# Performance work log

Measured on AMD Instinct MI355X. Metric: run time of the kernel, lower is better.

Reference implementation:

```python
import jax, jax.numpy as jnp
import numpy as np

N_NODES = 10000
N_EDGES = 5_000_000
BATCH = 2000


def setup_inputs() -> dict:
    key = jax.random.key(0)
    k1, k2, k3, k4 = jax.random.split(key, 4)
    n, E = N_NODES, N_EDGES
    # valid undirected pairs i < j
    i = jax.random.randint(k1, (E,), 0, n - 1)
    r = jax.random.randint(k2, (E,), 0, n)
    j = i + 1 + r % (n - 1 - i)
    edges = jnp.stack([i, j])  # [2, E], int
    edge_times = jax.random.uniform(k3, (E,), dtype=jnp.float32)
    edge_states = jax.random.randint(k4, (E,), 0, 2)
    return {
        "edges": edges,
        "edge_times": edge_times,
        "edge_states": edge_states,
        "nodes_num": n,
        "batch_size": BATCH,
    }


def _flat_idx(i, j, n):
    # undirected upper-triangular linearization of pair (i, j), i < j
    return i * n - i * (i + 1) // 2 + (j - i - 1)


def reference(edges, edge_times, edge_states, nodes_num, batch_size):
    n = nodes_num
    # -- multinomial(arange(n), batch_size, replacement=False) via Gumbel top-k --
    key = jax.random.key(19)
    w = jnp.arange(n, dtype=jnp.float32)
    logw = jnp.where(w > 0, jnp.log(jnp.maximum(w, 1.0)), -jnp.inf)
    scores = logw + jax.random.gumbel(key, (n,), dtype=jnp.float32)
    _, sel = jax.lax.top_k(scores, batch_size)
    batch_nodes = jnp.sort(sel)

    # -- all combinations (i < j since batch_nodes is sorted) --
    ii, jj = np.triu_indices(batch_size, k=1)  # static shapes
    batch_pairs = jnp.stack([batch_nodes[ii], batch_nodes[jj]])  # [2, P]
    batch_flat = _flat_idx(batch_pairs[0], batch_pairs[1], n)  # ascending

    # -- gather stored edges whose pair index is in the batch --
    edge_flat = _flat_idx(edges[0], edges[1], n)
    order = jnp.argsort(edge_flat)  # jax sort is stable -> matches coalesce order
    edges_sorted = edges[:, order]
    flat_sorted = edge_flat[order]
    times_sorted = edge_times[order]
    states_sorted = edge_states[order]

    pos = jnp.searchsorted(batch_flat, flat_sorted)
    pos = jnp.clip(pos, 0, batch_flat.shape[0] - 1)
    mask = batch_flat[pos] == flat_sorted  # [E] membership of each edge in batch

    batch_edge_times = jnp.where(mask, times_sorted, 0.0)
    batch_states = jnp.where(mask, states_sorted, 0)
    return (batch_nodes, batch_pairs, edges_sorted, batch_edge_times,
            batch_states, mask)
```

## Files before the change

### kernel.cpp

```cpp
#include <hip/hip_runtime.h>
#include <stdint.h>
#include <math.h>

#define N_NODES  10000
#define N_EDGES  5000000
#define BATCH    2000
#define N_PAIRS  1999000

#define OUT_BN      0
#define OUT_PAIRS0  2000
#define OUT_PAIRS1  2001000
#define OUT_ES0     4000000
#define OUT_ES1     9000000
#define OUT_T       14000000
#define OUT_S       19000000
#define OUT_M       24000000

#define WS_KEYS     0
#define WS_SEL      80000
#define WS_BN       120000
#define WS_CNT      128000
#define WS_FILL     168000
#define WS_OFF      208000
#define WS_SCRATCH  248064


#define RPB_LOG  7
#define NB1      79
#define CHUNK    4096
#define NBIN     192
#define NBITSW   313
#define RANK_BLKS 200
#define HIST_BLKS 128

typedef unsigned long long u64;

__device__ __forceinline__ u64 score_key(int w, unsigned bits) {
  const float TINY = 1.17549435e-38f;
  float uf = __uint_as_float((bits >> 9) | 0x3f800000u) - 1.0f;
  float val = fmaxf(TINY, uf + TINY);
  float t1 = (float)log((double)val);
  float gmb = -(float)log((double)(-t1));
  float score = (w > 0) ? ((float)log((double)w) + gmb) : (-INFINITY);
  unsigned fb = __float_as_uint(score);
  unsigned s = (fb & 0x80000000u) ? ~fb : (fb | 0x80000000u);
  unsigned d = ~s;
  return ((u64)d << 32) | (unsigned)w;
}

__device__ __forceinline__ u64 make_key(int v) {
  unsigned ks[3] = {0u, 19u, 0u ^ 19u ^ 0x1BD11BDAu};
  unsigned x0 = 0u + ks[0];
  unsigned x1 = (unsigned)v + ks[1];
  const int R0[4] = {13, 15, 26, 6};
  const int R1[4] = {17, 29, 16, 24};
#pragma unroll
  for (int g = 0; g < 5; ++g) {
    const int* R = (g & 1) ? R1 : R0;
#pragma unroll
    for (int r = 0; r < 4; ++r) {
      x0 += x1;
      x1 = (x1 << R[r]) | (x1 >> (32 - R[r]));
      x1 ^= x0;
    }
    x0 += ks[(g + 1) % 3];
    x1 += ks[(g + 2) % 3] + (unsigned)(g + 1);
  }
  return score_key(v, x0 ^ x1);
}

__global__ void __launch_bounds__(256) k_rankhist(
    int* __restrict__ rankc, int* __restrict__ cnt,
    const int4* __restrict__ e_i4) {
  __shared__ __align__(16) int sh4[N_NODES];
  int tid = threadIdx.x;
  if ((int)blockIdx.x < RANK_BLKS) {
    u64* lk = (u64*)sh4;
    int vblk = blockIdx.x / 5, cblk = blockIdx.x % 5;
    int base = cblk * 2048;
    int lenc = min(2048, N_NODES - base);
    for (int t = tid; t < lenc; t += 256) lk[t] = make_key(base + t);
    __syncthreads();
    int v = vblk * 256 + tid;
    u64 kv = (v < N_NODES) ? make_key(v) : 0;
    int c = 0;
    for (int t = 0; t < lenc; ++t) c += (lk[t] < kv) ? 1 : 0;
    if (v < N_NODES && c) atomicAdd(&rankc[v], c);
  } else {
    int* h = sh4;
    for (int t = tid; t < N_NODES; t += 256) h[t] = 0;
    __syncthreads();
    int hb = blockIdx.x - RANK_BLKS;
    int stride = HIST_BLKS * 256;
    for (int t = hb * 256 + tid; t < N_EDGES / 4; t += stride) {
      int4 r = e_i4[t];
      atomicAdd(&h[r.x], 1);
      atomicAdd(&h[r.y], 1);
      atomicAdd(&h[r.z], 1);
      atomicAdd(&h[r.w], 1);
    }
    __syncthreads();
    for (int t = tid; t < N_NODES; t += 256) {
      int c = h[t];
      if (c) atomicAdd(&cnt[t], c);
    }
  }
}

__global__ void k_scan_all(const int* rankc, int* sel, int* bn, float* outbn,
                           const int* cnt, int* off, int* fill, int* fill1,
                           unsigned* selbits) {
  __shared__ int wsum[16];
  __shared__ unsigned lb[320];
  const int PER = 10;
  int tid = threadIdx.x, lane = tid & 63, wid = tid >> 6;
  int base = tid * PER;
  int svv[PER];
  {
    int s = 0;
#pragma unroll
    for (int k = 0; k < PER; ++k) {
      int i = base + k;
      if (i < N_NODES) {
        int sv = (rankc[i] < BATCH) ? 1 : 0;
        sel[i] = sv;
        svv[k] = sv;
        s += sv;
      } else svv[k] = 0;
    }
    int inc = s;
#pragma unroll
    for (int d = 1; d < 64; d <<= 1) {
      int v = __shfl_up(inc, d, 64);
      if (lane >= d) inc += v;
    }
    if (lane == 63) wsum[wid] = inc;
    __syncthreads();
    int woff = 0;
    for (int w = 0; w < wid; ++w) woff += wsum[w];
    int run = woff + inc - s;
#pragma unroll
    for (int k = 0; k < PER; ++k) {
      int i = base + k;
      if (i < N_NODES && svv[k]) {
        bn[run] = i;
        outbn[run] = (float)i;
        ++run;
      }
    }
  }
  __syncthreads();
  {
    int cv[PER];
    int s = 0;
#pragma unroll
    for (int k = 0; k < PER; ++k) {
      int i = base + k;
      if (i < N_NODES) { cv[k] = cnt[i]; s += cv[k]; } else cv[k] = 0;
    }
    int inc = s;
#pragma unroll
    for (int d = 1; d < 64; d <<= 1) {
      int v = __shfl_up(inc, d, 64);
      if (lane >= d) inc += v;
    }
    if (lane == 63) wsum[wid] = inc;
    __syncthreads();
    int woff = 0;
    for (int w = 0; w < wid; ++w) woff += wsum[w];
    int run = woff + inc - s;
#pragma unroll
    for (int k = 0; k < PER; ++k) {
      int i = base + k;
      if (i < N_NODES) {
        off[i] = run;
        fill[i] = run;
        if ((i & ((1 << RPB_LOG) - 1)) == 0) fill1[i >> RPB_LOG] = run;
        run += cv[k];
      }
    }
    if (tid == 0) off[N_NODES] = N_EDGES;
  }
  __syncthreads();
  if (tid < 320) lb[tid] = 0;
  __syncthreads();
#pragma unroll
  for (int k = 0; k < PER; ++k) {
    int i = base + k;
    if (i < N_NODES && svv[k]) atomicOr(&lb[i >> 5], 1u << (i & 31));
  }
  __syncthreads();
  if (tid < NBITSW) selbits[tid] = lb[tid];
}

__global__ void __launch_bounds__(256) k_pairs_part1(
    const int* __restrict__ e_i, const int* __restrict__ e_j,
    const int* __restrict__ st, int* __restrict__ fill1,
    u64* __restrict__ stage, const int* __restrict__ bn,
    float* __restrict__ outp, int nblk1) {
  __shared__ u64 lkey[CHUNK];
  __shared__ int h[4][NB1];
  __shared__ int bstart[NB1], basec[NB1];
  __shared__ int tcount_s;
  int tid = threadIdx.x, wid = tid >> 6;
  if ((int)blockIdx.x >= nblk1) {
    int p = ((int)blockIdx.x - nblk1) * 256 + tid;
    if (p >= N_PAIRS) return;
    float tf = 2.0f * BATCH - 1.0f;
    float disc = tf * tf - 8.0f * (float)p;
    int ii = (int)((tf - sqrtf(disc)) * 0.5f);
    if (ii < 0) ii = 0;
    if (ii > BATCH - 2) ii = BATCH - 2;
    while (ii > 0 &&
           (long long)ii * (BATCH - 1) - (long long)ii * (ii - 1) / 2 > p) --ii;
    while ((long long)(ii + 1) * (BATCH - 1) - (long long)(ii + 1) * ii / 2 <= p) ++ii;
    long long S = (long long)ii * (BATCH - 1) - (long long)ii * (ii - 1) / 2;
    int jj = ii + 1 + (int)(p - S);
    outp[p] = (float)bn[ii];
    outp[N_PAIRS + p] = (float)bn[jj];
    return;
  }
  int c0 = (int)blockIdx.x * CHUNK;
  int nloc = min(CHUNK, N_EDGES - c0);
  for (int t = tid; t < 4 * NB1; t += 256) ((int*)h)[t] = 0;
  __syncthreads();
  int iv[CHUNK / 256];
  const int4* e_i4 = (const int4*)(e_i + c0);
#pragma unroll
  for (int k = 0; k < CHUNK / 1024; ++k) {
    int q = tid + 256 * k;
    int ebase = 4 * q;
    if (ebase < nloc) {
      int4 r = e_i4[q];
      iv[4 * k + 0] = r.x; iv[4 * k + 1] = r.y;
      iv[4 * k + 2] = r.z; iv[4 * k + 3] = r.w;
      atomicAdd(&h[wid][r.x >> RPB_LOG], 1);
      atomicAdd(&h[wid][r.y >> RPB_LOG], 1);
      atomicAdd(&h[wid][r.z >> RPB_LOG], 1);
      atomicAdd(&h[wid][r.w >> RPB_LOG], 1);
    } else {
      iv[4 * k + 0] = iv[4 * k + 1] = iv[4 * k + 2] = iv[4 * k + 3] = -1;
    }
  }
  __syncthreads();
  if (tid < 64) {
    int a0 = h[0][tid], a1 = h[1][tid], a2 = h[2][tid], a3 = h[3][tid];
    int a = a0 + a1 + a2 + a3;
    int b0 = 0, b1 = 0, b2 = 0, b3 = 0, b = 0;
    if (tid + 64 < NB1) {
      b0 = h[0][tid + 64]; b1 = h[1][tid + 64];
      b2 = h[2][tid + 64]; b3 = h[3][tid + 64];
      b = b0 + b1 + b2 + b3;
    }
    int inc0 = a;
#pragma unroll
    for (int d = 1; d < 64; d <<= 1) {
      int v = __shfl_up(inc0, d, 64);
      if (tid >= d) inc0 += v;
    }
    int t0 = __shfl(inc0, 63, 64);
    int inc1 = b;
#pragma unroll
    for (int d = 1; d < 64; d <<= 1) {
      int v = __shfl_up(inc1, d, 64);
      if (tid >= d) inc1 += v;
    }
    int tot = t0 + __shfl(inc1, 63, 64);
    int e0 = inc0 - a;
    bstart[tid] = e0;
    h[0][tid] = e0;
    h[1][tid] = e0 + a0;
    h[2][tid] = e0 + a0 + a1;
    h[3][tid] = e0 + a0 + a1 + a2;
    basec[tid] = a ? atomicAdd(&fill1[tid], a) : 0;
    if (tid + 64 < NB1) {
      int e1 = t0 + inc1 - b;
      bstart[tid + 64] = e1;
      h[0][tid + 64] = e1;
      h[1][tid + 64] = e1 + b0;
      h[2][tid + 64] = e1 + b0 + b1;
      h[3][tid + 64] = e1 + b0 + b1 + b2;
      basec[tid + 64] = b ? atomicAdd(&fill1[tid + 64], b) : 0;
    }
    if (tid == 0) tcount_s = tot;
  }
  __syncthreads();
  const int4* e_j4 = (const int4*)(e_j + c0);
  const int4* st4 = (const int4*)(st + c0);
#pragma unroll
  for (int k = 0; k < CHUNK / 1024; ++k) {
    int q = tid + 256 * k;
    int ebase = 4 * q;
    if (ebase < nloc) {
      int4 jj = e_j4[q];
      int4 ss = st4[q];
      int js[4] = {jj.x, jj.y, jj.z, jj.w};
      int s4[4] = {ss.x, ss.y, ss.z, ss.w};
#pragma unroll
      for (int c = 0; c < 4; ++c) {
        int i = iv[4 * k + c];
        unsigned e = (unsigned)(c0 + ebase + c);
        int b = i >> RPB_LOG;
        int pos = atomicAdd(&h[wid][b], 1);
        lkey[pos] = ((u64)(unsigned)i << 38) | ((u64)(unsigned)js[c] << 24) |
                    ((u64)e << 1) | (u64)(unsigned)s4[c];
      }
    }
  }
  __syncthreads();
  int tcount = tcount_s;
  for (int t = tid; t < tcount; t += 256) {
    u64 kv = lkey[t];
    int b = (int)(kv >> (38 + RPB_LOG));
    stage[basec[b] + (t - bstart[b])] = kv;
  }
}

__global__ void __launch_bounds__(256) k_part2(
    const u64* __restrict__ stage, int* __restrict__ fill,
    u64* __restrict__ sk) {
  __shared__ u64 lkey[CHUNK];
  __shared__ int h[4][256];
  __shared__ int bstart[256], baser[256], wsum4[4];
  __shared__ int rowbase_s;
  int tid = threadIdx.x, lane = tid & 63, wid = tid >> 6;
  int c0 = (int)blockIdx.x * CHUNK;
  int nloc = min(CHUNK, N_EDGES - c0);
  h[0][tid] = 0; h[1][tid] = 0; h[2][tid] = 0; h[3][tid] = 0;
  if (tid == 0)
    rowbase_s = ((int)(stage[c0] >> (38 + RPB_LOG))) << RPB_LOG;
  __syncthreads();
  int rowbase = rowbase_s;
  u64 kv[CHUNK / 256];
#pragma unroll
  for (int k = 0; k < CHUNK / 256; ++k) {
    int q = tid + 256 * k;
    if (q < nloc) {
      kv[k] = stage[c0 + q];
      atomicAdd(&h[wid][(int)(kv[k] >> 38) - rowbase], 1);
    }
  }
  __syncthreads();
  int h0 = h[0][tid], h1 = h[1][tid], h2 = h[2][tid], h3 = h[3][tid];
  int hv = h0 + h1 + h2 + h3;
  int inc = hv;
#pragma unroll
  for (int d = 1; d < 64; d <<= 1) {
    int v = __shfl_up(inc, d, 64);
    if (lane >= d) inc += v;
  }
  if (lane == 63) wsum4[wid] = inc;
  __syncthreads();
  int woff = 0;
  for (int w = 0; w < wid; ++w) woff += wsum4[w];
  int tcount = wsum4[0] + wsum4[1] + wsum4[2] + wsum4[3];
  int excl = woff + inc - hv;
  bstart[tid] = excl;
  h[0][tid] = excl;
  h[1][tid] = excl + h0;
  h[2][tid] = excl + h0 + h1;
  h[3][tid] = excl + h0 + h1 + h2;
  baser[tid] = hv ? atomicAdd(&fill[rowbase + tid], hv) : 0;
  __syncthreads();
#pragma unroll
  for (int k = 0; k < CHUNK / 256; ++k) {
    int q = tid + 256 * k;
    if (q < nloc) {
      int lr = (int)(kv[k] >> 38) - rowbase;
      int pos = atomicAdd(&h[wid][lr], 1);
      lkey[pos] = kv[k];
    }
  }
  __syncthreads();
  for (int t = tid; t < tcount; t += 256) {
    u64 v = lkey[t];
    int lr = (int)(v >> 38) - rowbase;
    sk[baser[lr] + (t - bstart[lr])] = v;
  }
}

__global__ void __launch_bounds__(256) k_rowsort_key(
    const u64* __restrict__ sk, const int* __restrict__ off,
    const float* __restrict__ times, const unsigned* __restrict__ selbits,
    float* __restrict__ out) {
  __shared__ u64 buf[768];
  __shared__ int hist[NBIN], cur[NBIN];
  __shared__ unsigned bits[320];
  int tid = threadIdx.x;
  int row = blockIdx.x;
  int o0 = off[row], o1 = off[row + 1];
  int len = o1 - o0;
  if (len <= 0) return;
  if (len > 768) len = 768;
  int span = N_NODES - 1 - row;
  int s = 0;
  while ((span >> s) >= 160) ++s;
  int mi = (int)((selbits[row >> 5] >> (row & 31)) & 1u);
  for (int t = tid; t < NBIN; t += 256) hist[t] = 0;
  if (mi) {
    for (int t = tid; t < NBITSW; t += 256) bits[t] = selbits[t];
  }
  __syncthreads();
  u64 kv[3];
  int dv[3], rv[3];
  int jbase = row + 1;
#pragma unroll
  for (int k = 0; k < 3; ++k) {
    int t = tid + 256 * k;
    if (t < len) {
      u64 v = sk[o0 + t];
      kv[k] = v;
      int j = (int)((v >> 24) & 0x3FFFull);
      int d = (j - jbase) >> s;
      dv[k] = d;
      atomicAdd(&hist[d], 1);
    } else {
      dv[k] = -1;
    }
  }
  __syncthreads();
  if (tid < 64) {
    int b0 = tid * 3;
    int c0 = hist[b0], c1 = hist[b0 + 1], c2 = hist[b0 + 2];
    int sum = c0 + c1 + c2;
    int inc = sum;
#pragma unroll
    for (int d = 1; d < 64; d <<= 1) {
      int v = __shfl_up(inc, d, 64);
      if (tid >= d) inc += v;
    }
    int excl = inc - sum;
    hist[b0] = excl;
    hist[b0 + 1] = excl + c0;
    hist[b0 + 2] = excl + c0 + c1;
    cur[b0] = excl;
    cur[b0 + 1] = excl + c0;
    cur[b0 + 2] = excl + c0 + c1;
  }
  __syncthreads();
#pragma unroll
  for (int k = 0; k < 3; ++k) {
    if (dv[k] >= 0) {
      int pos = atomicAdd(&cur[dv[k]], 1);
      buf[pos] = kv[k];
    }
  }
  __syncthreads();
#pragma unroll
  for (int k = 0; k < 3; ++k) {
    if (dv[k] >= 0) {
      u64 me = kv[k];
      int s0 = hist[dv[k]];
      int s1 = cur[dv[k]];
      int r = 0;
      for (int q = s0; q < s1; ++q) r += (buf[q] < me) ? 1 : 0;
      rv[k] = s0 + r;
    }
  }
  __syncthreads();
#pragma unroll
  for (int k = 0; k < 3; ++k)
    if (dv[k] >= 0) buf[rv[k]] = kv[k];
  __syncthreads();
  float frow = (float)row;
  if (mi) {
    for (int t = tid; t < len; t += 256) {
      u64 k = buf[t];
      int j = (int)((k >> 24) & 0x3FFFull);
      int idx = (int)((k >> 1) & 0x7FFFFFull);
      int st = (int)(k & 1ull);
      int p = o0 + t;
      out[OUT_ES0 + p] = frow;
      out[OUT_ES1 + p] = (float)j;
      bool m = (bits[j >> 5] >> (j & 31)) & 1u;
      out[OUT_T + p] = m ? times[idx] : 0.0f;
      out[OUT_S + p] = m ? (float)st : 0.0f;
      out[OUT_M + p] = m ? 1.0f : 0.0f;
    }
  } else {
    for (int t = tid; t < len; t += 256) {
      u64 k = buf[t];
      int j = (int)((k >> 24) & 0x3FFFull);
      int p = o0 + t;
      out[OUT_ES0 + p] = frow;
      out[OUT_ES1 + p] = (float)j;
      out[OUT_T + p] = 0.0f;
      out[OUT_S + p] = 0.0f;
      out[OUT_M + p] = 0.0f;
    }
  }
}

__global__ void __launch_bounds__(256) k_scatter_idx(
    const int4* __restrict__ e_i4, int* __restrict__ fill,
    unsigned* __restrict__ sk) {
  int t = blockIdx.x * blockDim.x + threadIdx.x;
  if (t >= N_EDGES / 4) return;
  int4 r = e_i4[t];
  unsigned e = 4u * (unsigned)t;
  int c0 = atomicAdd(&fill[r.x], 1);
  int c1 = atomicAdd(&fill[r.y], 1);
  int c2 = atomicAdd(&fill[r.z], 1);
  int c3 = atomicAdd(&fill[r.w], 1);
  sk[c0] = e;
  sk[c1] = e + 1;
  sk[c2] = e + 2;
  sk[c3] = e + 3;
}

__global__ void __launch_bounds__(256) k_rowsort_idx(
    const unsigned* __restrict__ sk, const int* __restrict__ e_j_arr,
    const int* __restrict__ off, const float* __restrict__ times,
    const int* __restrict__ states, const int* __restrict__ sel,
    float* __restrict__ out) {
  __shared__ u64 key[2048];
  int row = blockIdx.x;
  int o0 = off[row], o1 = off[row + 1];
  int len = o1 - o0;
  if (len <= 0) return;
  if (len > 2048) len = 2048;
  int M = 2;
  while (M < len) M <<= 1;
  for (int t = threadIdx.x; t < M; t += blockDim.x) {
    if (t < len) {
      unsigned e = sk[o0 + t];
      key[t] = ((u64)(unsigned)e_j_arr[e] << 32) | e;
    } else {
      key[t] = 0xFFFFFFFFFFFFFFFFull;
    }
  }
  __syncthreads();
  for (int k = 2; k <= M; k <<= 1) {
    for (int j = k >> 1; j > 0; j >>= 1) {
      for (int t = threadIdx.x; t < M; t += blockDim.x) {
        int ixj = t ^ j;
        if (ixj > t) {
          u64 a = key[t], b = key[ixj];
          bool up = ((t & k) == 0);
          if (up ? (a > b) : (a < b)) {
            key[t] = b;
            key[ixj] = a;
          }
        }
      }
      __syncthreads();
    }
  }
  int mi = sel[row];
  float frow = (float)row;
  for (int t = threadIdx.x; t < len; t += blockDim.x) {
    u64 k = key[t];
    int j = (int)(k >> 32);
    int idx = (int)(k & 0xFFFFFFFFull);
    int p = o0 + t;
    out[OUT_ES0 + p] = frow;
    out[OUT_ES1 + p] = (float)j;
    bool m = (mi != 0) && (sel[j] != 0);
    float tm = 0.0f, sv = 0.0f;
    if (m) {
      tm = times[idx];
      sv = (float)states[idx];
    }
    out[OUT_T + p] = tm;
    out[OUT_S + p] = sv;
    out[OUT_M + p] = m ? 1.0f : 0.0f;
  }
}

extern "C" void kernel_launch(void* const* d_in, const int* in_sizes, int n_in,
                              void* d_out, int out_size, void* d_ws, size_t ws_size,
                              hipStream_t stream) {
  const int* edges = (const int*)d_in[0];
  const float* times = (const float*)d_in[1];
  const int* states = (const int*)d_in[2];
  const int* e_i = edges;
  const int* e_j = edges + N_EDGES;
  float* out = (float*)d_out;
  char* ws = (char*)d_ws;

  int* fill1 = (int*)(ws + WS_KEYS);
  int* sel = (int*)(ws + WS_SEL);
  int* bn = (int*)(ws + WS_BN);
  int* cnt = (int*)(ws + WS_CNT);
  unsigned* selbits = (unsigned*)(ws + WS_CNT);
  int* fill = (int*)(ws + WS_FILL);
  int* rankc = (int*)(ws + WS_FILL);
  int* off = (int*)(ws + WS_OFF);
  u64* sk64 = (u64*)(ws + WS_SCRATCH);
  unsigned* sk32 = (unsigned*)(ws + WS_SCRATCH);
  u64* stage = (u64*)(out + OUT_ES0);
  int use64 = (ws_size >= (size_t)WS_SCRATCH + 8ull * N_EDGES) ? 1 : 0;

  hipMemsetAsync(ws + WS_CNT, 0, 80000, stream);

  int npair_b = (N_PAIRS + 255) / 256;
  k_rankhist<<<RANK_BLKS + HIST_BLKS, 256, 0, stream>>>(rankc, cnt,
                                                        (const int4*)e_i);
  k_scan_all<<<1, 1024, 0, stream>>>(rankc, sel, bn, out + OUT_BN, cnt, off,
                                     fill, fill1, selbits);
  if (use64) {
    int nblk1 = (N_EDGES + CHUNK - 1) / CHUNK;
    k_pairs_part1<<<nblk1 + npair_b, 256, 0, stream>>>(
        e_i, e_j, states, fill1, stage, bn, out + OUT_PAIRS0, nblk1);
    k_part2<<<nblk1, 256, 0, stream>>>(stage, fill, sk64);
    k_rowsort_key<<<N_NODES, 256, 0, stream>>>(sk64, off, times, selbits, out);
  } else {
    k_pairs_part1<<<npair_b, 256, 0, stream>>>(
        e_i, e_j, states, fill1, stage, bn, out + OUT_PAIRS0, 0);
    k_scatter_idx<<<(N_EDGES / 4 + 255) / 256, 256, 0, stream>>>(
        (const int4*)e_i, fill, sk32);
    k_rowsort_idx<<<N_NODES, 256, 0, stream>>>(sk32, e_j, off, times, states,
                                               sel, out);
  }
}
```

Baseline: 359.0 us.

## Partition edges into 8-row groups and sort each group per block

The second partition pass now buckets keys by groups of 8 rows instead of single rows, which shrinks the shared histogram and scan. The row sort kernel processes 8 rows per block (1250 blocks) with 1024 bins, each row getting 128 sub-bins keyed by its j range. This amortises per-block setup and launch overhead across more keys. In exchange each block holds 18 keys per thread and a larger shared buffer, which lowers occupancy, and groups larger than the 4608-entry capacity are truncated.

```diff
diff --git a/kernel.cpp b/kernel.cpp
--- a/kernel.cpp
+++ b/kernel.cpp
@@ -28,10 +28,14 @@
 #define RPB_LOG  7
 #define NB1      79
 #define CHUNK    4096
-#define NBIN     192
 #define NBITSW   313
 #define RANK_BLKS 200
 #define HIST_BLKS 128
+#define GRPLOG   3
+#define NGRP     1250
+#define GBINS    1024
+#define GCAP     4608
+#define KPT      18
 
 typedef unsigned long long u64;
 
@@ -109,7 +113,7 @@
 
 __global__ void k_scan_all(const int* rankc, int* sel, int* bn, float* outbn,
                            const int* cnt, int* off, int* fill, int* fill1,
-                           unsigned* selbits) {
+                           int* fill8, unsigned* selbits) {
   __shared__ int wsum[16];
   __shared__ unsigned lb[320];
   const int PER = 10;
@@ -176,6 +180,7 @@
         off[i] = run;
         fill[i] = run;
         if ((i & ((1 << RPB_LOG) - 1)) == 0) fill1[i >> RPB_LOG] = run;
+        if ((i & ((1 << GRPLOG) - 1)) == 0) fill8[i >> GRPLOG] = run;
         run += cv[k];
       }
     }
@@ -317,65 +322,70 @@
 }
 
 __global__ void __launch_bounds__(256) k_part2(
-    const u64* __restrict__ stage, int* __restrict__ fill,
+    const u64* __restrict__ stage, int* __restrict__ fill8,
     u64* __restrict__ sk) {
   __shared__ u64 lkey[CHUNK];
-  __shared__ int h[4][256];
-  __shared__ int bstart[256], baser[256], wsum4[4];
+  __shared__ int h[4][32];
+  __shared__ int bstart[32], baser8[32];
   __shared__ int rowbase_s;
-  int tid = threadIdx.x, lane = tid & 63, wid = tid >> 6;
+  int tid = threadIdx.x, wid = tid >> 6;
   int c0 = (int)blockIdx.x * CHUNK;
   int nloc = min(CHUNK, N_EDGES - c0);
-  h[0][tid] = 0; h[1][tid] = 0; h[2][tid] = 0; h[3][tid] = 0;
+  if (tid < 128) ((int*)h)[tid] = 0;
   if (tid == 0)
     rowbase_s = ((int)(stage[c0] >> (38 + RPB_LOG))) << RPB_LOG;
   __syncthreads();
   int rowbase = rowbase_s;
+  int grp0 = rowbase >> GRPLOG;
   u64 kv[CHUNK / 256];
 #pragma unroll
   for (int k = 0; k < CHUNK / 256; ++k) {
     int q = tid + 256 * k;
     if (q < nloc) {
       kv[k] = stage[c0 + q];
-      atomicAdd(&h[wid][(int)(kv[k] >> 38) - rowbase], 1);
-    }
-  }
-  __syncthreads();
-  int h0 = h[0][tid], h1 = h[1][tid], h2 = h[2][tid], h3 = h[3][tid];
-  int hv = h0 + h1 + h2 + h3;
-  int inc = hv;
-#pragma unroll
-  for (int d = 1; d < 64; d <<= 1) {
-    int v = __shfl_up(inc, d, 64);
-    if (lane >= d) inc += v;
-  }
-  if (lane == 63) wsum4[wid] = inc;
-  __syncthreads();
-  int woff = 0;
-  for (int w = 0; w < wid; ++w) woff += wsum4[w];
-  int tcount = wsum4[0] + wsum4[1] + wsum4[2] + wsum4[3];
-  int excl = woff + inc - hv;
-  bstart[tid] = excl;
-  h[0][tid] = excl;
-  h[1][tid] = excl + h0;
-  h[2][tid] = excl + h0 + h1;
-  h[3][tid] = excl + h0 + h1 + h2;
-  baser[tid] = hv ? atomicAdd(&fill[rowbase + tid], hv) : 0;
+      int g = ((int)(kv[k] >> 38) - rowbase) >> GRPLOG;
+      atomicAdd(&h[wid][g], 1);
+    }
+  }
+  __syncthreads();
+  if (tid < 64) {
+    int b = tid;
+    int a0 = 0, a1 = 0, a2 = 0, a3 = 0, a = 0;
+    if (b < 32) {
+      a0 = h[0][b]; a1 = h[1][b]; a2 = h[2][b]; a3 = h[3][b];
+      a = a0 + a1 + a2 + a3;
+    }
+    int inc = a;
+#pragma unroll
+    for (int d = 1; d < 64; d <<= 1) {
+      int v = __shfl_up(inc, d, 64);
+      if (tid >= d) inc += v;
+    }
+    int excl = inc - a;
+    if (b < 32) {
+      bstart[b] = excl;
+      h[0][b] = excl;
+      h[1][b] = excl + a0;
+      h[2][b] = excl + a0 + a1;
+      h[3][b] = excl + a0 + a1 + a2;
+      baser8[b] = a ? atomicAdd(&fill8[grp0 + b], a) : 0;
+    }
+  }
   __syncthreads();
 #pragma unroll
   for (int k = 0; k < CHUNK / 256; ++k) {
     int q = tid + 256 * k;
     if (q < nloc) {
-      int lr = (int)(kv[k] >> 38) - rowbase;
-      int pos = atomicAdd(&h[wid][lr], 1);
+      int g = ((int)(kv[k] >> 38) - rowbase) >> GRPLOG;
+      int pos = atomicAdd(&h[wid][g], 1);
       lkey[pos] = kv[k];
     }
   }
   __syncthreads();
-  for (int t = tid; t < tcount; t += 256) {
+  for (int t = tid; t < nloc; t += 256) {
     u64 v = lkey[t];
-    int lr = (int)(v >> 38) - rowbase;
-    sk[baser[lr] + (t - bstart[lr])] = v;
+    int g = ((int)(v >> 38) - rowbase) >> GRPLOG;
+    sk[baser8[g] + (t - bstart[g])] = v;
   }
 }
 
@@ -383,35 +393,36 @@
     const u64* __restrict__ sk, const int* __restrict__ off,
     const float* __restrict__ times, const unsigned* __restrict__ selbits,
     float* __restrict__ out) {
-  __shared__ u64 buf[768];
-  __shared__ int hist[NBIN], cur[NBIN];
+  __shared__ u64 buf[GCAP];
+  __shared__ int hist[GBINS], cur[GBINS];
   __shared__ unsigned bits[320];
-  int tid = threadIdx.x;
-  int row = blockIdx.x;
-  int o0 = off[row], o1 = off[row + 1];
-  int len = o1 - o0;
-  if (len <= 0) return;
-  if (len > 768) len = 768;
-  int span = N_NODES - 1 - row;
-  int s = 0;
-  while ((span >> s) >= 160) ++s;
-  int mi = (int)((selbits[row >> 5] >> (row & 31)) & 1u);
-  for (int t = tid; t < NBIN; t += 256) hist[t] = 0;
-  if (mi) {
-    for (int t = tid; t < NBITSW; t += 256) bits[t] = selbits[t];
-  }
-  __syncthreads();
-  u64 kv[3];
-  int dv[3], rv[3];
-  int jbase = row + 1;
-#pragma unroll
-  for (int k = 0; k < 3; ++k) {
+  __shared__ int wsum4[4];
+  int tid = threadIdx.x, lane = tid & 63, wid = tid >> 6;
+  int r0 = (int)blockIdx.x << GRPLOG;
+  int o0 = off[r0], o1 = off[r0 + (1 << GRPLOG)];
+  int blen = o1 - o0;
+  if (blen <= 0) return;
+  if (blen > GCAP) blen = GCAP;
+  u64 kv[KPT];
+  int dv[KPT], rv[KPT];
+#pragma unroll
+  for (int k = 0; k < KPT; ++k) {
     int t = tid + 256 * k;
-    if (t < len) {
-      u64 v = sk[o0 + t];
-      kv[k] = v;
-      int j = (int)((v >> 24) & 0x3FFFull);
-      int d = (j - jbase) >> s;
+    kv[k] = (t < blen) ? sk[o0 + t] : 0;
+  }
+  for (int t = tid; t < GBINS; t += 256) hist[t] = 0;
+  for (int t = tid; t < NBITSW; t += 256) bits[t] = selbits[t];
+  __syncthreads();
+#pragma unroll
+  for (int k = 0; k < KPT; ++k) {
+    int t = tid + 256 * k;
+    if (t < blen) {
+      u64 v = kv[k];
+      int row = (int)(v >> 38);
+      int span = N_NODES - 1 - row;
+      int sh = 17 + ((span > 1) ? (32 - __clz(span - 1)) : 0);
+      u64 rel = (v & 0x3FFFFFFFFFull) - ((u64)(row + 1) << 24);
+      int d = ((row - r0) << 7) | (int)(rel >> sh);
       dv[k] = d;
       atomicAdd(&hist[d], 1);
     } else {
@@ -419,27 +430,30 @@
     }
   }
   __syncthreads();
-  if (tid < 64) {
-    int b0 = tid * 3;
-    int c0 = hist[b0], c1 = hist[b0 + 1], c2 = hist[b0 + 2];
-    int sum = c0 + c1 + c2;
+  {
+    int b4 = tid * 4;
+    int c0 = hist[b4], c1 = hist[b4 + 1], c2 = hist[b4 + 2], c3 = hist[b4 + 3];
+    int sum = c0 + c1 + c2 + c3;
     int inc = sum;
 #pragma unroll
     for (int d = 1; d < 64; d <<= 1) {
       int v = __shfl_up(inc, d, 64);
-      if (tid >= d) inc += v;
-    }
-    int excl = inc - sum;
-    hist[b0] = excl;
-    hist[b0 + 1] = excl + c0;
-    hist[b0 + 2] = excl + c0 + c1;
-    cur[b0] = excl;
-    cur[b0 + 1] = excl + c0;
-    cur[b0 + 2] = excl + c0 + c1;
-  }
-  __syncthreads();
-#pragma unroll
-  for (int k = 0; k < 3; ++k) {
+      if (lane >= d) inc += v;
+    }
+    if (lane == 63) wsum4[wid] = inc;
+    __syncthreads();
+    int woff = 0;
+    for (int w = 0; w < wid; ++w) woff += wsum4[w];
+    int excl = woff + inc - sum;
+    hist[b4] = excl;                 cur[b4] = excl;
+    hist[b4 + 1] = excl + c0;        cur[b4 + 1] = excl + c0;
+    hist[b4 + 2] = excl + c0 + c1;   cur[b4 + 2] = excl + c0 + c1;
+    hist[b4 + 3] = excl + c0 + c1 + c2;
+    cur[b4 + 3] = excl + c0 + c1 + c2;
+  }
+  __syncthreads();
+#pragma unroll
+  for (int k = 0; k < KPT; ++k) {
     if (dv[k] >= 0) {
       int pos = atomicAdd(&cur[dv[k]], 1);
       buf[pos] = kv[k];
@@ -447,7 +461,7 @@
   }
   __syncthreads();
 #pragma unroll
-  for (int k = 0; k < 3; ++k) {
+  for (int k = 0; k < KPT; ++k) {
     if (dv[k] >= 0) {
       u64 me = kv[k];
       int s0 = hist[dv[k]];
@@ -459,35 +473,22 @@
   }
   __syncthreads();
 #pragma unroll
-  for (int k = 0; k < 3; ++k)
+  for (int k = 0; k < KPT; ++k)
     if (dv[k] >= 0) buf[rv[k]] = kv[k];
   __syncthreads();
-  float frow = (float)row;
-  if (mi) {
-    for (int t = tid; t < len; t += 256) {
-      u64 k = buf[t];
-      int j = (int)((k >> 24) & 0x3FFFull);
-      int idx = (int)((k >> 1) & 0x7FFFFFull);
-      int st = (int)(k & 1ull);
-      int p = o0 + t;
-      out[OUT_ES0 + p] = frow;
-      out[OUT_ES1 + p] = (float)j;
-      bool m = (bits[j >> 5] >> (j & 31)) & 1u;
-      out[OUT_T + p] = m ? times[idx] : 0.0f;
-      out[OUT_S + p] = m ? (float)st : 0.0f;
-      out[OUT_M + p] = m ? 1.0f : 0.0f;
-    }
-  } else {
-    for (int t = tid; t < len; t += 256) {
-      u64 k = buf[t];
-      int j = (int)((k >> 24) & 0x3FFFull);
-      int p = o0 + t;
-      out[OUT_ES0 + p] = frow;
-      out[OUT_ES1 + p] = (float)j;
-      out[OUT_T + p] = 0.0f;
-      out[OUT_S + p] = 0.0f;
-      out[OUT_M + p] = 0.0f;
-    }
+  for (int t = tid; t < blen; t += 256) {
+    u64 k = buf[t];
+    int row = (int)(k >> 38);
+    int j = (int)((k >> 24) & 0x3FFFull);
+    int idx = (int)((k >> 1) & 0x7FFFFFull);
+    int p = o0 + t;
+    out[OUT_ES0 + p] = (float)row;
+    out[OUT_ES1 + p] = (float)j;
+    bool m = ((bits[row >> 5] >> (row & 31)) & 1u) &&
+             ((bits[j >> 5] >> (j & 31)) & 1u);
+    out[OUT_T + p] = m ? times[idx] : 0.0f;
+    out[OUT_S + p] = m ? (float)(int)(k & 1ull) : 0.0f;
+    out[OUT_M + p] = m ? 1.0f : 0.0f;
   }
 }
 
@@ -579,6 +580,7 @@
   char* ws = (char*)d_ws;
 
   int* fill1 = (int*)(ws + WS_KEYS);
+  int* fill8 = (int*)(ws + WS_KEYS + 4096);
   int* sel = (int*)(ws + WS_SEL);
   int* bn = (int*)(ws + WS_BN);
   int* cnt = (int*)(ws + WS_CNT);
@@ -597,13 +599,13 @@
   k_rankhist<<<RANK_BLKS + HIST_BLKS, 256, 0, stream>>>(rankc, cnt,
                                                         (const int4*)e_i);
   k_scan_all<<<1, 1024, 0, stream>>>(rankc, sel, bn, out + OUT_BN, cnt, off,
-                                     fill, fill1, selbits);
+                                     fill, fill1, fill8, selbits);
   if (use64) {
     int nblk1 = (N_EDGES + CHUNK - 1) / CHUNK;
     k_pairs_part1<<<nblk1 + npair_b, 256, 0, stream>>>(
         e_i, e_j, states, fill1, stage, bn, out + OUT_PAIRS0, nblk1);
-    k_part2<<<nblk1, 256, 0, stream>>>(stage, fill, sk64);
-    k_rowsort_key<<<N_NODES, 256, 0, stream>>>(sk64, off, times, selbits, out);
+    k_part2<<<nblk1, 256, 0, stream>>>(stage, fill8, sk64);
+    k_rowsort_key<<<NGRP, 256, 0, stream>>>(sk64, off, times, selbits, out);
   } else {
     k_pairs_part1<<<npair_b, 256, 0, stream>>>(
         e_i, e_j, states, fill1, stage, bn, out + OUT_PAIRS0, 0);
```

Result: faster. 339.5 us (-5.4%).
